# Kernel tuning notes

Measured on AMD Instinct MI355X. Metric: run time of the kernel, lower is better.

Reference implementation:

```python
import jax, jax.numpy as jnp
import numpy as np

N = 100000
E = 1600000
IN = 128
HID = 32
HEADS = 4
HID2 = 8  # hidden_channels / 4
OUT = 1


def setup_inputs() -> dict:
    key = jax.random.key(0)
    ks = jax.random.split(key, 13)
    def glorot(k, shape):
        fan = sum(shape[-2:]) if len(shape) >= 2 else shape[-1]
        return jax.random.normal(k, shape, dtype=jnp.float32) * (2.0 / fan) ** 0.5
    return {
        "x": jax.random.normal(ks[0], (N, IN), dtype=jnp.float32),
        "edge_index": jax.random.randint(ks[1], (2, E), 0, N, dtype=jnp.int32),
        "edge_attr": jax.random.normal(ks[2], (E, 8), dtype=jnp.float32),  # ignored by GATConv (edge_dim=None)
        "W1": glorot(ks[3], (IN, HEADS * HID)),
        "a_src1": glorot(ks[4], (HEADS, HID)),
        "a_dst1": glorot(ks[5], (HEADS, HID)),
        "b1": jnp.zeros((HEADS * HID,), dtype=jnp.float32),
        "W2": glorot(ks[6], (HEADS * HID, 1 * HID2)),
        "a_src2": glorot(ks[7], (1, HID2)),
        "a_dst2": glorot(ks[8], (1, HID2)),
        "b2": jnp.zeros((HID2,), dtype=jnp.float32),
        "Wlin": glorot(ks[9], (HID2, OUT)),
        "blin": jnp.zeros((OUT,), dtype=jnp.float32),
    }


def gat_layer(x, W, a_src, a_dst, bias, src, dst, num_nodes, concat):
    """PyG GATConv (edge_dim=None): gather -> LeakyReLU attn -> segment softmax over dst -> scatter-add."""
    H, C = a_src.shape
    h = (x @ W).reshape(num_nodes, H, C)                        # [N, H, C]
    alpha_s = jnp.einsum('nhc,hc->nh', h, a_src)                # [N, H]
    alpha_d = jnp.einsum('nhc,hc->nh', h, a_dst)
    e = jax.nn.leaky_relu(alpha_s[src] + alpha_d[dst], 0.2)     # [E, H]
    m = jax.ops.segment_max(e, dst, num_segments=num_nodes)     # softmax over incoming edges per dst
    ex = jnp.exp(e - m[dst])
    denom = jax.ops.segment_sum(ex, dst, num_segments=num_nodes)
    alpha = ex / (denom[dst] + 1e-16)                           # [E, H]
    out = jax.ops.segment_sum(h[src] * alpha[:, :, None], dst, num_segments=num_nodes)  # [N, H, C]
    out = out.reshape(num_nodes, H * C) if concat else out.mean(axis=1)
    return out + bias


def reference(x, edge_index, edge_attr, W1, a_src1, a_dst1, b1, W2, a_src2, a_dst2, b2, Wlin, blin):
    n = x.shape[0]
    loops = jnp.arange(n, dtype=edge_index.dtype)               # add_self_loops=True (PyG default)
    src = jnp.concatenate([edge_index[0], loops])
    dst = jnp.concatenate([edge_index[1], loops])
    h = jax.nn.elu(gat_layer(x, W1, a_src1, a_dst1, b1, src, dst, n, True))
    h = jax.nn.elu(gat_layer(h, W2, a_src2, a_dst2, b2, src, dst, n, False))
    return jax.nn.sigmoid(h @ Wlin + blin)                      # [N, 1]
```

## Files before the change

### kernel.cpp

```cpp
#include <hip/hip_runtime.h>
#include <hip/hip_bf16.h>

__device__ __forceinline__ float lrelu02(float v) { return v > 0.f ? v : 0.2f * v; }

__device__ __forceinline__ float bf2f(unsigned short u) {
    union { unsigned int i; float f; } v; v.i = ((unsigned int)u) << 16; return v.f;
}
__device__ __forceinline__ unsigned short f2bf(float f) {
    union { float f; unsigned int i; } v; v.f = f;
    unsigned int x = v.i;
    return (unsigned short)((x + 0x7fffu + ((x >> 16) & 1u)) >> 16);
}

__global__ __launch_bounds__(256) void gemm1_k(
    const float* __restrict__ x, const float* __restrict__ W1,
    const float* __restrict__ aw_s, const float* __restrict__ aw_d,
    unsigned short* __restrict__ h1b, float* __restrict__ as1, float* __restrict__ ad1, int N)
{
    __shared__ float Wl[128 * 128];
    for (int i = threadIdx.x; i < 128 * 128 / 4; i += 256)
        ((float4*)Wl)[i] = ((const float4*)W1)[i];

    const int cl = threadIdx.x & 15;
    const int rg = threadIdx.x >> 4;
    const int head = cl >> 2;
    const int row0 = blockIdx.x * 64 + rg * 4;
    __syncthreads();

    const float4* x4[4];
    bool rv[4];
    #pragma unroll
    for (int r = 0; r < 4; ++r) {
        int rr = row0 + r;
        rv[r] = rr < N;
        int rc = rv[r] ? rr : (N - 1);
        x4[r] = (const float4*)(x + (size_t)rc * 128);
    }

    float acc[4][8];
    #pragma unroll
    for (int r = 0; r < 4; ++r)
        #pragma unroll
        for (int c = 0; c < 8; ++c) acc[r][c] = 0.f;

    for (int k4 = 0; k4 < 32; ++k4) {
        float4 xv[4];
        #pragma unroll
        for (int r = 0; r < 4; ++r) xv[r] = x4[r][k4];
        #pragma unroll
        for (int kk = 0; kk < 4; ++kk) {
            const int k = k4 * 4 + kk;
            const float4 w0 = *(const float4*)(Wl + k * 128 + cl * 8);
            const float4 w1 = *(const float4*)(Wl + k * 128 + cl * 8 + 4);
            #pragma unroll
            for (int r = 0; r < 4; ++r) {
                const float xk = kk == 0 ? xv[r].x : kk == 1 ? xv[r].y : kk == 2 ? xv[r].z : xv[r].w;
                acc[r][0] = fmaf(xk, w0.x, acc[r][0]);
                acc[r][1] = fmaf(xk, w0.y, acc[r][1]);
                acc[r][2] = fmaf(xk, w0.z, acc[r][2]);
                acc[r][3] = fmaf(xk, w0.w, acc[r][3]);
                acc[r][4] = fmaf(xk, w1.x, acc[r][4]);
                acc[r][5] = fmaf(xk, w1.y, acc[r][5]);
                acc[r][6] = fmaf(xk, w1.z, acc[r][6]);
                acc[r][7] = fmaf(xk, w1.w, acc[r][7]);
            }
        }
    }

    float ws_[8], wd_[8];
    #pragma unroll
    for (int c = 0; c < 8; ++c) { ws_[c] = aw_s[cl * 8 + c]; wd_[c] = aw_d[cl * 8 + c]; }

    #pragma unroll
    for (int r = 0; r < 4; ++r) {
        float s = 0.f, d = 0.f;
        #pragma unroll
        for (int c = 0; c < 8; ++c) { s = fmaf(acc[r][c], ws_[c], s); d = fmaf(acc[r][c], wd_[c], d); }
        s += __shfl_xor(s, 1); s += __shfl_xor(s, 2);
        d += __shfl_xor(d, 1); d += __shfl_xor(d, 2);
        if (rv[r]) {
            if ((cl & 3) == 0) { as1[(row0 + r) * 4 + head] = s; ad1[(row0 + r) * 4 + head] = d; }
            uint4 pk;
            pk.x = f2bf(acc[r][0]) | ((unsigned)f2bf(acc[r][1]) << 16);
            pk.y = f2bf(acc[r][2]) | ((unsigned)f2bf(acc[r][3]) << 16);
            pk.z = f2bf(acc[r][4]) | ((unsigned)f2bf(acc[r][5]) << 16);
            pk.w = f2bf(acc[r][6]) | ((unsigned)f2bf(acc[r][7]) << 16);
            *(uint4*)(h1b + (size_t)(row0 + r) * 128 + cl * 8) = pk;
        }
    }
}

__global__ __launch_bounds__(256) void rank_k(
    const int* __restrict__ ei, int E, int N,
    int* __restrict__ deg, int* __restrict__ rank)
{
    int e = blockIdx.x * 256 + threadIdx.x;
    if (e >= E + N) return;
    int d = (e < E) ? ei[E + e] : (e - E);
    rank[e] = atomicAdd(&deg[d], 1);
}

__global__ __launch_bounds__(256) void blocksum_k(
    const int* __restrict__ deg, int N, int* __restrict__ bsum)
{
    __shared__ int sh[256];
    int i = blockIdx.x * 256 + threadIdx.x;
    sh[threadIdx.x] = (i < N) ? deg[i] : 0;
    __syncthreads();
    for (int off = 128; off; off >>= 1) {
        if (threadIdx.x < off) sh[threadIdx.x] += sh[threadIdx.x + off];
        __syncthreads();
    }
    if (threadIdx.x == 0) bsum[blockIdx.x] = sh[0];
}

__global__ __launch_bounds__(1024) void scanbsum_k(int* __restrict__ bsum, int nb)
{
    __shared__ int buf[1024];
    __shared__ int carry;
    if (threadIdx.x == 0) carry = 0;
    __syncthreads();
    for (int base = 0; base < nb; base += 1024) {
        int i = base + threadIdx.x;
        int v = (i < nb) ? bsum[i] : 0;
        buf[threadIdx.x] = v;
        __syncthreads();
        for (int off = 1; off < 1024; off <<= 1) {
            int t = (threadIdx.x >= off) ? buf[threadIdx.x - off] : 0;
            __syncthreads();
            buf[threadIdx.x] += t;
            __syncthreads();
        }
        if (i < nb) bsum[i] = buf[threadIdx.x] - v + carry;
        __syncthreads();
        if (threadIdx.x == 0) carry += buf[1023];
        __syncthreads();
    }
}

__global__ __launch_bounds__(256) void rowptr_k(
    const int* __restrict__ deg, const int* __restrict__ bsum, int N, int E,
    int* __restrict__ rowptr)
{
    __shared__ int buf[256];
    int i = blockIdx.x * 256 + threadIdx.x;
    int v = (i < N) ? deg[i] : 0;
    buf[threadIdx.x] = v;
    __syncthreads();
    for (int off = 1; off < 256; off <<= 1) {
        int t = (threadIdx.x >= off) ? buf[threadIdx.x - off] : 0;
        __syncthreads();
        buf[threadIdx.x] += t;
        __syncthreads();
    }
    if (i < N) rowptr[i] = bsum[blockIdx.x] + buf[threadIdx.x] - v;
    if (i == 0) rowptr[N] = E + N;
}

__global__ __launch_bounds__(256) void place_k(
    const int* __restrict__ ei, int E, int N,
    const int* __restrict__ rank, const int* __restrict__ rowptr,
    int* __restrict__ csr)
{
    int e = blockIdx.x * 256 + threadIdx.x;
    if (e >= E + N) return;
    int s, d;
    if (e < E) { s = ei[e]; d = ei[E + e]; } else { s = d = e - E; }
    csr[rowptr[d] + rank[e]] = s;
}

__global__ __launch_bounds__(256) void gat1_k(
    const int* __restrict__ csr, const int* __restrict__ rowptr,
    const float* __restrict__ as1, const float* __restrict__ ad1,
    const unsigned short* __restrict__ h1b, const float* __restrict__ b1,
    unsigned short* __restrict__ out1b, int N)
{
    const int wid  = (blockIdx.x * 256 + threadIdx.x) >> 6;
    const int lane = threadIdx.x & 63;
    if (wid >= N) return;
    const int start = rowptr[wid], end = rowptr[wid + 1];
    const int i16 = lane & 15;
    const int hh  = lane >> 4;
    const float adh = ad1[wid * 4 + hh];
    const float mh  = lrelu02(as1[wid * 4 + hh] + adh);
    const unsigned short* hb = h1b + lane * 2;

    float den = 0.f, acc0 = 0.f, acc1 = 0.f;
    int k0 = start;
    for (; k0 + 16 <= end; k0 += 16) {
        int s = csr[k0 + i16];
        float w = __expf(lrelu02(as1[s * 4 + hh] + adh) - mh);
        den += w;
        #pragma unroll
        for (int e = 0; e < 16; ++e) {
            int se = __builtin_amdgcn_readlane(s, e);
            float we = __shfl(w, e, 16);
            unsigned int pv = *(const unsigned int*)(hb + (size_t)se * 128);
            acc0 = fmaf(bf2f((unsigned short)pv), we, acc0);
            acc1 = fmaf(bf2f((unsigned short)(pv >> 16)), we, acc1);
        }
    }
    int cnt = end - k0;
    if (cnt > 0) {
        int s = (i16 < cnt) ? csr[k0 + i16] : wid;
        float w = (i16 < cnt) ? __expf(lrelu02(as1[s * 4 + hh] + adh) - mh) : 0.f;
        den += w;
        for (int e = 0; e < cnt; ++e) {
            int se = __builtin_amdgcn_readlane(s, e);
            float we = __shfl(w, e, 16);
            unsigned int pv = *(const unsigned int*)(hb + (size_t)se * 128);
            acc0 = fmaf(bf2f((unsigned short)pv), we, acc0);
            acc1 = fmaf(bf2f((unsigned short)(pv >> 16)), we, acc1);
        }
    }
    den += __shfl_xor(den, 1); den += __shfl_xor(den, 2);
    den += __shfl_xor(den, 4); den += __shfl_xor(den, 8);
    const float rden = 1.f / (den + 1e-16f);
    float v0 = acc0 * rden + b1[lane * 2];
    float v1 = acc1 * rden + b1[lane * 2 + 1];
    v0 = v0 > 0.f ? v0 : expm1f(v0);
    v1 = v1 > 0.f ? v1 : expm1f(v1);
    *(unsigned int*)(out1b + (size_t)wid * 128 + lane * 2) =
        f2bf(v0) | ((unsigned)f2bf(v1) << 16);
}

__global__ __launch_bounds__(256) void gemm2_k(
    const unsigned short* __restrict__ h2b, const float* __restrict__ W2,
    const float* __restrict__ aw_s, const float* __restrict__ aw_d,
    float* __restrict__ g, float* __restrict__ as2, float* __restrict__ ad2, int N)
{
    __shared__ float W2l[128 * 8];
    __shared__ float rows[32][129];
    for (int i = threadIdx.x; i < 128 * 8; i += 256) W2l[i] = W2[i];
    const int r = threadIdx.x >> 3, j = threadIdx.x & 7;
    const float ws_ = aw_s[j], wd_ = aw_d[j];
    for (int base = blockIdx.x * 32; base < N; base += gridDim.x * 32) {
        __syncthreads();
        for (int i = threadIdx.x; i < 32 * 64; i += 256) {
            int rr = i >> 6, kp = i & 63;
            int n = base + rr;
            unsigned int pv = (n < N) ? *(const unsigned int*)(h2b + (size_t)n * 128 + kp * 2) : 0u;
            rows[rr][kp * 2]     = bf2f((unsigned short)pv);
            rows[rr][kp * 2 + 1] = bf2f((unsigned short)(pv >> 16));
        }
        __syncthreads();
        int n = base + r;
        float acc = 0.f;
        #pragma unroll
        for (int k = 0; k < 128; ++k) acc += rows[r][k] * W2l[k * 8 + j];
        if (n < N) {
            g[n * 8 + j] = acc;
            float s = acc * ws_, d = acc * wd_;
            #pragma unroll
            for (int off = 4; off; off >>= 1) {
                s += __shfl_down(s, off, 8);
                d += __shfl_down(d, off, 8);
            }
            if (j == 0) { as2[n] = s; ad2[n] = d; }
        }
    }
}

__global__ __launch_bounds__(256) void gat2_k(
    const int* __restrict__ csr, const int* __restrict__ rowptr,
    const float* __restrict__ as2, const float* __restrict__ ad2,
    const float* __restrict__ g, const float* __restrict__ b2_,
    const float* __restrict__ Wlin, const float* __restrict__ blin,
    float* __restrict__ out, int N)
{
    const int wid  = (blockIdx.x * 256 + threadIdx.x) >> 6;
    const int lane = threadIdx.x & 63;
    if (wid >= N) return;
    const int start = rowptr[wid], end = rowptr[wid + 1];
    const int i8  = lane & 7;
    const int grp = lane >> 3;
    const float adh = ad2[wid];
    const float mh  = lrelu02(as2[wid] + adh);
    float den = 0.f, acc = 0.f;
    int k0 = start;
    for (; k0 + 8 <= end; k0 += 8) {
        int s = csr[k0 + i8];
        float w = __expf(lrelu02(as2[s] + adh) - mh);
        den += w;
        int   se = __shfl(s, grp, 8);
        float we = __shfl(w, grp, 8);
        acc = fmaf(we, g[(size_t)se * 8 + i8], acc);
    }
    int cnt = end - k0;
    if (cnt > 0) {
        int s = (i8 < cnt) ? csr[k0 + i8] : wid;
        float w = (i8 < cnt) ? __expf(lrelu02(as2[s] + adh) - mh) : 0.f;
        den += w;
        int   se = __shfl(s, grp, 8);
        float we = __shfl(w, grp, 8);
        acc = fmaf(we, g[(size_t)se * 8 + i8], acc);
    }
    den += __shfl_xor(den, 1); den += __shfl_xor(den, 2); den += __shfl_xor(den, 4);
    acc += __shfl_xor(acc, 8); acc += __shfl_xor(acc, 16); acc += __shfl_xor(acc, 32);
    float v = acc / (den + 1e-16f) + b2_[i8];
    v = v > 0.f ? v : expm1f(v);
    float t = v * Wlin[i8];
    t += __shfl_xor(t, 1); t += __shfl_xor(t, 2); t += __shfl_xor(t, 4);
    if (lane == 0) out[wid] = 1.f / (1.f + __expf(-(t + blin[0])));
}

extern "C" void kernel_launch(void* const* d_in, const int* in_sizes, int n_in,
                              void* d_out, int out_size, void* d_ws, size_t ws_size,
                              hipStream_t stream)
{
    (void)n_in; (void)out_size; (void)ws_size;
    const float* x    = (const float*)d_in[0];
    const int*   ei   = (const int*)d_in[1];
    const float* W1   = (const float*)d_in[3];
    const float* as1w = (const float*)d_in[4];
    const float* ad1w = (const float*)d_in[5];
    const float* b1   = (const float*)d_in[6];
    const float* W2   = (const float*)d_in[7];
    const float* as2w = (const float*)d_in[8];
    const float* ad2w = (const float*)d_in[9];
    const float* b2v  = (const float*)d_in[10];
    const float* Wlin = (const float*)d_in[11];
    const float* blin = (const float*)d_in[12];

    const int N = in_sizes[0] / 128;
    const int E = in_sizes[1] / 2;
    const int total = E + N;

    float* p = (float*)d_ws;
    unsigned short* h1b   = (unsigned short*)p; p += (size_t)N * 64;
    unsigned short* out1b = (unsigned short*)p; p += (size_t)N * 64;
    float* as1  = p; p += (size_t)N * 4;
    float* ad1  = p; p += (size_t)N * 4;
    float* g    = p; p += (size_t)N * 8;
    float* as2  = p; p += (size_t)N;
    float* ad2  = p; p += (size_t)N;
    int* deg    = (int*)p; p += (size_t)N;
    int* rowptr = (int*)p; p += (size_t)N + 1;
    int* bsum   = (int*)p; p += ((size_t)N + 255) / 256;
    int* rank   = (int*)p; p += (size_t)total;
    int* csr    = (int*)p; p += (size_t)total;

    const int eb = (total + 255) / 256;
    const int nb = (N + 255) / 256;

    hipMemsetAsync(deg, 0, (size_t)N * sizeof(int), stream);
    gemm1_k<<<(N + 63) / 64, 256, 0, stream>>>(x, W1, as1w, ad1w, h1b, as1, ad1, N);
    rank_k<<<eb, 256, 0, stream>>>(ei, E, N, deg, rank);
    blocksum_k<<<nb, 256, 0, stream>>>(deg, N, bsum);
    scanbsum_k<<<1, 1024, 0, stream>>>(bsum, nb);
    rowptr_k<<<nb, 256, 0, stream>>>(deg, bsum, N, E, rowptr);
    place_k<<<eb, 256, 0, stream>>>(ei, E, N, rank, rowptr, csr);

    gat1_k<<<(N * 64 + 255) / 256, 256, 0, stream>>>(csr, rowptr, as1, ad1, h1b, b1, out1b, N);

    gemm2_k<<<3125, 256, 0, stream>>>(out1b, W2, as2w, ad2w, g, as2, ad2, N);
    gat2_k<<<(N * 64 + 255) / 256, 256, 0, stream>>>(csr, rowptr, as2, ad2, g, b2v, Wlin, blin,
                                                     (float*)d_out, N);
}
```

Before: 486.5 us.

## Fuse layer-2 projection into gat1 epilogue and degree counting into gemm1

The separate gemm2 kernel is removed. Each gat1 wavefront now multiplies its ELU output row by W2 in registers, reduces across lanes with shuffles plus a small LDS buffer, and writes g, as2 and ad2 directly. This removes the bf16 out1b intermediate write and re-read and one kernel launch. The rank/degree atomic pass is also folded into gemm1 as a grid-stride prologue, which drops another launch but puts atomic work in front of each GEMM block. The cross-lane LDS exchange has no barrier and relies on wavefront lockstep.

```diff
diff --git a/kernel.cpp b/kernel.cpp
--- a/kernel.cpp
+++ b/kernel.cpp
@@ -15,8 +15,18 @@
 __global__ __launch_bounds__(256) void gemm1_k(
     const float* __restrict__ x, const float* __restrict__ W1,
     const float* __restrict__ aw_s, const float* __restrict__ aw_d,
-    unsigned short* __restrict__ h1b, float* __restrict__ as1, float* __restrict__ ad1, int N)
-{
+    unsigned short* __restrict__ h1b, float* __restrict__ as1, float* __restrict__ ad1, int N,
+    const int* __restrict__ ei, int E, int* __restrict__ deg, int* __restrict__ rank)
+{
+    {
+        const int total = E + N;
+        const int stride = gridDim.x * 256;
+        for (int e = blockIdx.x * 256 + threadIdx.x; e < total; e += stride) {
+            int d = (e < E) ? ei[E + e] : (e - E);
+            rank[e] = atomicAdd(&deg[d], 1);
+        }
+    }
+
     __shared__ float Wl[128 * 128];
     for (int i = threadIdx.x; i < 128 * 128 / 4; i += 256)
         ((float4*)Wl)[i] = ((const float4*)W1)[i];
@@ -90,16 +100,6 @@
     }
 }
 
-__global__ __launch_bounds__(256) void rank_k(
-    const int* __restrict__ ei, int E, int N,
-    int* __restrict__ deg, int* __restrict__ rank)
-{
-    int e = blockIdx.x * 256 + threadIdx.x;
-    if (e >= E + N) return;
-    int d = (e < E) ? ei[E + e] : (e - E);
-    rank[e] = atomicAdd(&deg[d], 1);
-}
-
 __global__ __launch_bounds__(256) void blocksum_k(
     const int* __restrict__ deg, int N, int* __restrict__ bsum)
 {
@@ -173,8 +173,11 @@
     const int* __restrict__ csr, const int* __restrict__ rowptr,
     const float* __restrict__ as1, const float* __restrict__ ad1,
     const unsigned short* __restrict__ h1b, const float* __restrict__ b1,
-    unsigned short* __restrict__ out1b, int N)
-{
+    const float* __restrict__ W2, const float* __restrict__ aw_s2, const float* __restrict__ aw_d2,
+    float* __restrict__ g, float* __restrict__ as2, float* __restrict__ ad2, int N)
+{
+    __shared__ float red[4][8][12];
+    const int wv   = threadIdx.x >> 6;
     const int wid  = (blockIdx.x * 256 + threadIdx.x) >> 6;
     const int lane = threadIdx.x & 63;
     if (wid >= N) return;
@@ -220,44 +223,35 @@
     float v1 = acc1 * rden + b1[lane * 2 + 1];
     v0 = v0 > 0.f ? v0 : expm1f(v0);
     v1 = v1 > 0.f ? v1 : expm1f(v1);
-    *(unsigned int*)(out1b + (size_t)wid * 128 + lane * 2) =
-        f2bf(v0) | ((unsigned)f2bf(v1) << 16);
-}
-
-__global__ __launch_bounds__(256) void gemm2_k(
-    const unsigned short* __restrict__ h2b, const float* __restrict__ W2,
-    const float* __restrict__ aw_s, const float* __restrict__ aw_d,
-    float* __restrict__ g, float* __restrict__ as2, float* __restrict__ ad2, int N)
-{
-    __shared__ float W2l[128 * 8];
-    __shared__ float rows[32][129];
-    for (int i = threadIdx.x; i < 128 * 8; i += 256) W2l[i] = W2[i];
-    const int r = threadIdx.x >> 3, j = threadIdx.x & 7;
-    const float ws_ = aw_s[j], wd_ = aw_d[j];
-    for (int base = blockIdx.x * 32; base < N; base += gridDim.x * 32) {
-        __syncthreads();
-        for (int i = threadIdx.x; i < 32 * 64; i += 256) {
-            int rr = i >> 6, kp = i & 63;
-            int n = base + rr;
-            unsigned int pv = (n < N) ? *(const unsigned int*)(h2b + (size_t)n * 128 + kp * 2) : 0u;
-            rows[rr][kp * 2]     = bf2f((unsigned short)pv);
-            rows[rr][kp * 2 + 1] = bf2f((unsigned short)(pv >> 16));
-        }
-        __syncthreads();
-        int n = base + r;
-        float acc = 0.f;
-        #pragma unroll
-        for (int k = 0; k < 128; ++k) acc += rows[r][k] * W2l[k * 8 + j];
-        if (n < N) {
-            g[n * 8 + j] = acc;
-            float s = acc * ws_, d = acc * wd_;
-            #pragma unroll
-            for (int off = 4; off; off >>= 1) {
-                s += __shfl_down(s, off, 8);
-                d += __shfl_down(d, off, 8);
-            }
-            if (j == 0) { as2[n] = s; ad2[n] = d; }
-        }
+
+    const float4 a0 = *(const float4*)(W2 + 16 * lane);
+    const float4 a1 = *(const float4*)(W2 + 16 * lane + 4);
+    const float4 b0 = *(const float4*)(W2 + 16 * lane + 8);
+    const float4 b1v = *(const float4*)(W2 + 16 * lane + 12);
+    float p[8];
+    p[0] = v0 * a0.x + v1 * b0.x;  p[1] = v0 * a0.y + v1 * b0.y;
+    p[2] = v0 * a0.z + v1 * b0.z;  p[3] = v0 * a0.w + v1 * b0.w;
+    p[4] = v0 * a1.x + v1 * b1v.x; p[5] = v0 * a1.y + v1 * b1v.y;
+    p[6] = v0 * a1.z + v1 * b1v.z; p[7] = v0 * a1.w + v1 * b1v.w;
+    #pragma unroll
+    for (int j = 0; j < 8; ++j) {
+        p[j] += __shfl_xor(p[j], 8);
+        p[j] += __shfl_xor(p[j], 16);
+        p[j] += __shfl_xor(p[j], 32);
+    }
+    if (lane < 8) {
+        #pragma unroll
+        for (int j = 0; j < 8; ++j) red[wv][lane][j] = p[j];
+    }
+    if (lane < 8) {
+        float gj = 0.f;
+        #pragma unroll
+        for (int c = 0; c < 8; ++c) gj += red[wv][c][lane];
+        g[(size_t)wid * 8 + lane] = gj;
+        float ts = gj * aw_s2[lane], td = gj * aw_d2[lane];
+        ts += __shfl_xor(ts, 1); ts += __shfl_xor(ts, 2); ts += __shfl_xor(ts, 4);
+        td += __shfl_xor(td, 1); td += __shfl_xor(td, 2); td += __shfl_xor(td, 4);
+        if (lane == 0) { as2[wid] = ts; ad2[wid] = td; }
     }
 }
 
@@ -327,8 +321,7 @@
     const int total = E + N;
 
     float* p = (float*)d_ws;
-    unsigned short* h1b   = (unsigned short*)p; p += (size_t)N * 64;
-    unsigned short* out1b = (unsigned short*)p; p += (size_t)N * 64;
+    unsigned short* h1b = (unsigned short*)p; p += (size_t)N * 64;
     float* as1  = p; p += (size_t)N * 4;
     float* ad1  = p; p += (size_t)N * 4;
     float* g    = p; p += (size_t)N * 8;
@@ -344,16 +337,15 @@
     const int nb = (N + 255) / 256;
 
     hipMemsetAsync(deg, 0, (size_t)N * sizeof(int), stream);
-    gemm1_k<<<(N + 63) / 64, 256, 0, stream>>>(x, W1, as1w, ad1w, h1b, as1, ad1, N);
-    rank_k<<<eb, 256, 0, stream>>>(ei, E, N, deg, rank);
+    gemm1_k<<<(N + 63) / 64, 256, 0, stream>>>(x, W1, as1w, ad1w, h1b, as1, ad1, N,
+                                               ei, E, deg, rank);
     blocksum_k<<<nb, 256, 0, stream>>>(deg, N, bsum);
     scanbsum_k<<<1, 1024, 0, stream>>>(bsum, nb);
     rowptr_k<<<nb, 256, 0, stream>>>(deg, bsum, N, E, rowptr);
     place_k<<<eb, 256, 0, stream>>>(ei, E, N, rank, rowptr, csr);
 
-    gat1_k<<<(N * 64 + 255) / 256, 256, 0, stream>>>(csr, rowptr, as1, ad1, h1b, b1, out1b, N);
-
-    gemm2_k<<<3125, 256, 0, stream>>>(out1b, W2, as2w, ad2w, g, as2, ad2, N);
+    gat1_k<<<(N * 64 + 255) / 256, 256, 0, stream>>>(csr, rowptr, as1, ad1, h1b, b1,
+                                                     W2, as2w, ad2w, g, as2, ad2, N);
     gat2_k<<<(N * 64 + 255) / 256, 256, 0, stream>>>(csr, rowptr, as2, ad2, g, b2v, Wlin, blin,
                                                      (float*)d_out, N);
 }
```

Result: faster. 447.0 us (-8.1%).
